# Kernel optimization log

Hardware: AMD Instinct MI355X
Metric: run time of the kernel (lower is better)

Reference implementation:

```python
import jax, jax.numpy as jnp
import numpy as np
from jax import lax

COMMITMENT_WEIGHT = 0.25
EMA_DECAY = 0.99
EPS = 1e-5


def setup_inputs() -> dict:
    key = jax.random.key(0)
    k1, k2, k3 = jax.random.split(key, 3)
    B, L, D, K = 32, 512, 384, 8192
    z = jax.random.normal(k1, (B, L, D), dtype=jnp.float32)
    codebook = jax.random.normal(k2, (K, D), dtype=jnp.float32)
    ema_cluster_size = jnp.zeros((K,), dtype=jnp.float32)
    ema_embed_sum = jax.random.normal(k3, (K, D), dtype=jnp.float32)
    return {"z": z, "codebook": codebook, "ema_cluster_size": ema_cluster_size, "ema_embed_sum": ema_embed_sum}


def reference(z, codebook, ema_cluster_size, ema_embed_sum):
    B, L, D = z.shape
    K = codebook.shape[0]
    flat_z = z.reshape(-1, D)  # [N, D]

    # squared L2 distance to every code: [N, K]
    dist = (
        jnp.sum(flat_z * flat_z, axis=-1, keepdims=True)
        + jnp.sum(codebook * codebook, axis=-1)[None, :]
        - 2.0 * (flat_z @ codebook.T)
    )
    indices = jnp.argmin(dist, axis=-1)  # [N]
    quantized = codebook[indices].reshape(B, L, D)

    # EMA codebook update (training-mode, no-grad in original)
    cluster_size = jax.ops.segment_sum(jnp.ones_like(indices, dtype=flat_z.dtype), indices, num_segments=K)
    embed_sum = jax.ops.segment_sum(flat_z, indices, num_segments=K)  # [K, D]
    new_cluster_size = ema_cluster_size * EMA_DECAY + (1.0 - EMA_DECAY) * cluster_size
    new_embed_sum = ema_embed_sum * EMA_DECAY + (1.0 - EMA_DECAY) * embed_sum
    n = jnp.sum(new_cluster_size)
    cluster_size_smoothed = (new_cluster_size + EPS) / (n + K * EPS) * n
    new_codebook = new_embed_sum / cluster_size_smoothed[:, None]

    commitment_loss = jnp.mean((z - lax.stop_gradient(quantized)) ** 2)
    codebook_loss = jnp.mean((quantized - lax.stop_gradient(z)) ** 2)
    loss = codebook_loss + COMMITMENT_WEIGHT * commitment_loss

    # straight-through estimator
    quantized_st = z + lax.stop_gradient(quantized - z)
    return (quantized_st, indices.reshape(B, L), loss, new_cluster_size, new_embed_sum, new_codebook)
```

## Files before the change

kernel.cpp:

```cpp
#include <hip/hip_runtime.h>
#include <math.h>

#define N_TOK 16384
#define DDIM  384
#define KCODE 8192
#define EMA   0.99f
#define EPS_F 1e-5f
#define MARGIN 0.5f
#define NB 32

typedef _Float16 f16x8 __attribute__((ext_vector_type(8)));
typedef float    f32x4 __attribute__((ext_vector_type(4)));

#define OFF_PD1    0UL
#define OFF_PI1    2097152UL
#define OFF_PD2    4194304UL
#define OFF_CBH    6291456UL
#define OFF_TOKL   0UL
#define OFF_OFFS   65536UL
#define OFF_CURS   98560UL
#define OFF_WSIDX  12582912UL
#define OFF_COUNTS 12648448UL
#define OFF_SUMSQ  12681216UL
#define OFF_NACC   12681220UL
#define OFF_CNORM  12681472UL
#define OFF_FLIST  12714240UL
#define OFF_FCNT   12779776UL
#define OFF_PSUM   12780032UL
#define OFF_FD1    12796416UL

typedef __attribute__((address_space(1))) const unsigned int gas_uint;
typedef __attribute__((address_space(3))) unsigned int       las_uint;
__device__ __forceinline__ void gload_lds16(const void* g, void* l) {
    __builtin_amdgcn_global_load_lds((gas_uint*)g, (las_uint*)l, 16, 0, 0);
}

__global__ void convert_norm_kernel(const float* __restrict__ z, const float* __restrict__ cb,
                                    _Float16* __restrict__ zh, _Float16* __restrict__ cbh,
                                    float* __restrict__ cnorm) {
    int row  = (blockIdx.x * blockDim.x + threadIdx.x) >> 6;
    int lane = threadIdx.x & 63;
    const float* src;
    _Float16* dst;
    bool is_cb = (row >= N_TOK);
    if (is_cb) { int k = row - N_TOK; src = cb + (size_t)k * DDIM; dst = cbh + (size_t)k * DDIM; }
    else       {                      src = z  + (size_t)row * DDIM; dst = zh + (size_t)row * DDIM; }
    float s = 0.f;
    #pragma unroll
    for (int r = 0; r < 3; r++) {
        int e = (lane + 64 * r) * 2;
        float2 v = *(const float2*)(src + e);
        s = fmaf(v.x, v.x, fmaf(v.y, v.y, s));
        _Float16 h0 = (_Float16)v.x, h1 = (_Float16)v.y;
        dst[e] = h0; dst[e + 1] = h1;
    }
    if (is_cb) {
        #pragma unroll
        for (int off = 32; off > 0; off >>= 1) s += __shfl_down(s, off, 64);
        if (lane == 0) cnorm[row - N_TOK] = s;
    }
}

__launch_bounds__(512, 4)
__global__ void argmin16_kernel(const _Float16* __restrict__ zh, const _Float16* __restrict__ cbh,
                                const float* __restrict__ cnorm,
                                float* __restrict__ pd1, int* __restrict__ pi1,
                                float* __restrict__ pd2) {
    __shared__ _Float16 As[128 * 64];
    __shared__ _Float16 Bs[256 * 64];

    const int tid  = threadIdx.x;
    const int lane = tid & 63;
    const int wv   = tid >> 6;
    const int wy   = wv >> 2;
    const int wx   = wv & 3;
    const int m0   = blockIdx.x * 128;
    const int n0   = blockIdx.y * 256;
    const int l15  = lane & 15;
    const int l4   = lane >> 4;
    const int rsw  = l15 & 7;

    f32x4 acc[4][4];
    #pragma unroll
    for (int i = 0; i < 4; i++)
        #pragma unroll
        for (int j = 0; j < 4; j++) acc[i][j] = (f32x4){0.f, 0.f, 0.f, 0.f};

    const int r8  = lane >> 3;
    const int jch = (lane & 7) ^ (r8 & 7);
    const _Float16* a_g = zh  + (size_t)(m0 + wv * 8 + r8) * DDIM + jch * 8;
    const _Float16* b_g = cbh + (size_t)(n0 + wv * 8 + r8) * DDIM + jch * 8;
    _Float16* a_d = As + wv * 512;
    _Float16* b_d = Bs + wv * 512;

    gload_lds16(a_g,                      a_d);
    gload_lds16(a_g + (size_t)64 * DDIM,  a_d + 4096);
    gload_lds16(b_g,                      b_d);
    gload_lds16(b_g + (size_t)64 * DDIM,  b_d + 4096);
    gload_lds16(b_g + (size_t)128 * DDIM, b_d + 8192);
    gload_lds16(b_g + (size_t)192 * DDIM, b_d + 12288);

    for (int it = 0; it < 6; it++) {
        __syncthreads();
        f16x8 af[4], bf[4];
        #pragma unroll
        for (int im = 0; im < 4; im++)
            af[im] = *(const f16x8*)(As + (wy * 64 + im * 16 + l15) * 64 + (l4 ^ rsw) * 8);
        #pragma unroll
        for (int in = 0; in < 4; in++)
            bf[in] = *(const f16x8*)(Bs + (wx * 64 + in * 16 + l15) * 64 + (l4 ^ rsw) * 8);
        #pragma unroll
        for (int im = 0; im < 4; im++)
            #pragma unroll
            for (int in = 0; in < 4; in++)
                acc[im][in] = __builtin_amdgcn_mfma_f32_16x16x32_f16(af[im], bf[in], acc[im][in], 0, 0, 0);
        #pragma unroll
        for (int im = 0; im < 4; im++)
            af[im] = *(const f16x8*)(As + (wy * 64 + im * 16 + l15) * 64 + ((4 + l4) ^ rsw) * 8);
        #pragma unroll
        for (int in = 0; in < 4; in++)
            bf[in] = *(const f16x8*)(Bs + (wx * 64 + in * 16 + l15) * 64 + ((4 + l4) ^ rsw) * 8);
        __syncthreads();
        if (it < 5) {
            int kc = (it + 1) * 64;
            gload_lds16(a_g + kc,                      a_d);
            gload_lds16(a_g + (size_t)64 * DDIM + kc,  a_d + 4096);
            gload_lds16(b_g + kc,                      b_d);
            gload_lds16(b_g + (size_t)64 * DDIM + kc,  b_d + 4096);
            gload_lds16(b_g + (size_t)128 * DDIM + kc, b_d + 8192);
            gload_lds16(b_g + (size_t)192 * DDIM + kc, b_d + 12288);
        }
        #pragma unroll
        for (int im = 0; im < 4; im++)
            #pragma unroll
            for (int in = 0; in < 4; in++)
                acc[im][in] = __builtin_amdgcn_mfma_f32_16x16x32_f16(af[im], bf[in], acc[im][in], 0, 0, 0);
    }

    float* xd1 = (float*)&As[0];
    float* xd2 = xd1 + 512;
    int*   xi1 = (int*)(xd1 + 1024);

    float cn[4]; int cid[4];
    #pragma unroll
    for (int in = 0; in < 4; in++) {
        cid[in] = n0 + wx * 64 + in * 16 + l15;
        cn[in] = cnorm[cid[in]];
    }
    #pragma unroll
    for (int im = 0; im < 4; im++) {
        #pragma unroll
        for (int reg = 0; reg < 4; reg++) {
            float d1 = cn[0] - 2.f * acc[im][0][reg];
            int   i1 = cid[0];
            float d2 = 3.4e38f;
            #pragma unroll
            for (int in = 1; in < 4; in++) {
                float dd = cn[in] - 2.f * acc[im][in][reg];
                if (dd < d1) { d2 = d1; d1 = dd; i1 = cid[in]; }
                else d2 = fminf(d2, dd);
            }
            #pragma unroll
            for (int off = 1; off < 16; off <<= 1) {
                float od1 = __shfl_xor(d1, off, 16);
                int   oi1 = __shfl_xor(i1, off, 16);
                float od2 = __shfl_xor(d2, off, 16);
                if (od1 < d1 || (od1 == d1 && oi1 < i1)) { d2 = fminf(d1, od2); d1 = od1; i1 = oi1; }
                else d2 = fminf(d2, od1);
            }
            if (l15 == 0) {
                int tl = wy * 64 + im * 16 + l4 * 4 + reg;
                xd1[tl * 4 + wx] = d1; xi1[tl * 4 + wx] = i1; xd2[tl * 4 + wx] = d2;
            }
        }
    }
    __syncthreads();
    if (tid < 128) {
        float d1 = xd1[tid * 4], d2 = xd2[tid * 4];
        int   i1 = xi1[tid * 4];
        #pragma unroll
        for (int x = 1; x < 4; x++) {
            float od1 = xd1[tid * 4 + x], od2 = xd2[tid * 4 + x];
            int   oi1 = xi1[tid * 4 + x];
            if (od1 < d1 || (od1 == d1 && oi1 < i1)) { d2 = fminf(d1, od2); d1 = od1; i1 = oi1; }
            else d2 = fminf(d2, od1);
        }
        size_t o = (size_t)blockIdx.y * N_TOK + m0 + tid;
        pd1[o] = d1; pi1[o] = i1; pd2[o] = d2;
    }
}

__global__ void topmerge_kernel(const float* __restrict__ pd1, const int* __restrict__ pi1,
                                const float* __restrict__ pd2,
                                int* __restrict__ ws_idx, float* __restrict__ out_idx,
                                int* __restrict__ fcnt, int* __restrict__ flist,
                                float* __restrict__ fd1) {
    int t = blockIdx.x * blockDim.x + threadIdx.x;
    if (t >= N_TOK) return;
    float d1 = pd1[t], d2 = pd2[t];
    int   i1 = pi1[t];
    for (int nb = 1; nb < NB; nb++) {
        size_t o = (size_t)nb * N_TOK + t;
        float od1 = pd1[o], od2 = pd2[o];
        int   oi1 = pi1[o];
        if (od1 < d1 || (od1 == d1 && oi1 < i1)) { d2 = fminf(d1, od2); d1 = od1; i1 = oi1; }
        else d2 = fminf(d2, od1);
    }
    ws_idx[t] = i1;
    out_idx[t] = (float)i1;
    fd1[t] = d1;
    if (d2 - d1 < MARGIN) {
        int s = atomicAdd(fcnt, 1);
        flist[s] = t;
    }
}

__launch_bounds__(256)
__global__ void rescore2_kernel(const float* __restrict__ z, const float* __restrict__ cb,
                                const float* __restrict__ cnorm,
                                const float* __restrict__ pd1, const float* __restrict__ fd1,
                                const int* __restrict__ flist, const int* __restrict__ fcnt,
                                int* __restrict__ ws_idx, float* __restrict__ out_idx) {
    __shared__ float zt[4 * 384];
    const int lane = threadIdx.x & 63;
    const int wv   = threadIdx.x >> 6;
    const int count = fcnt[0];
    float* zrow = zt + wv * 384;
    for (int slot = blockIdx.x * 4 + wv; slot < count; slot += 2048 * 4) {
        int t = flist[slot];
        const float* zr = z + (size_t)t * DDIM;
        #pragma unroll
        for (int r = 0; r < 6; r++) zrow[lane + 64 * r] = zr[lane + 64 * r];
        float band = fd1[t] + MARGIN;
        float bd = 3.4e38f; int bi = 0x7fffffff;
        for (int nb = 0; nb < NB; nb++) {
            if (pd1[(size_t)nb * N_TOK + t] >= band) continue;
            #pragma unroll
            for (int c4 = 0; c4 < 4; c4++) {
                int c = nb * 256 + c4 * 64 + lane;
                const float* cr = cb + (size_t)c * DDIM;
                float a = 0.f;
                for (int d4 = 0; d4 < 96; d4++) {
                    float4 cv = *(const float4*)(cr + d4 * 4);
                    float4 zv = *(const float4*)(zrow + d4 * 4);
                    a = fmaf(zv.x, cv.x, a);
                    a = fmaf(zv.y, cv.y, a);
                    a = fmaf(zv.z, cv.z, a);
                    a = fmaf(zv.w, cv.w, a);
                }
                float dd = cnorm[c] - 2.f * a;
                if (dd < bd) { bd = dd; bi = c; }
            }
        }
        #pragma unroll
        for (int off = 32; off > 0; off >>= 1) {
            float od = __shfl_xor(bd, off, 64);
            int   oi = __shfl_xor(bi, off, 64);
            if (od < bd || (od == bd && oi < bi)) { bd = od; bi = oi; }
        }
        if (lane == 0) { ws_idx[t] = bi; out_idx[t] = (float)bi; }
    }
}

__global__ void quantize_kernel(const float* __restrict__ z, const float* __restrict__ cb,
                                const int* __restrict__ ws_idx,
                                float* __restrict__ out_q,
                                float* __restrict__ counts, float* __restrict__ psum) {
    __shared__ float sm[4];
    int t = (blockIdx.x * blockDim.x + threadIdx.x) >> 6;
    int lane = threadIdx.x & 63, wv = threadIdx.x >> 6;
    int k = ws_idx[t];
    const float* zr = z + (size_t)t * DDIM;
    const float* cr = cb + (size_t)k * DDIM;
    float* qr = out_q + (size_t)t * DDIM;
    float s = 0.f;
    #pragma unroll
    for (int r = 0; r < 6; r++) {
        int d = lane + 64 * r;
        float zv = zr[d];
        float qv = cr[d];
        qr[d] = qv;
        float df = zv - qv;
        s += df * df;
    }
    #pragma unroll
    for (int off = 32; off > 0; off >>= 1) s += __shfl_down(s, off, 64);
    if (lane == 0) {
        sm[wv] = s;
        atomicAdd(counts + k, 1.0f);
    }
    __syncthreads();
    if (threadIdx.x == 0) psum[blockIdx.x] = sm[0] + sm[1] + sm[2] + sm[3];
}

__global__ void scan_kernel(const float* __restrict__ counts,
                            int* __restrict__ offs, int* __restrict__ curs) {
    __shared__ int ps[1024];
    const int t = threadIdx.x;
    const int base = t * 8;
    int loc[8]; int s = 0;
    #pragma unroll
    for (int i = 0; i < 8; i++) { int c = (int)(counts[base + i] + 0.5f); loc[i] = s; s += c; }
    ps[t] = s;
    __syncthreads();
    for (int off = 1; off < 1024; off <<= 1) {
        int v = ps[t];
        int add = (t >= off) ? ps[t - off] : 0;
        __syncthreads();
        ps[t] = v + add;
        __syncthreads();
    }
    int excl = (t == 0) ? 0 : ps[t - 1];
    #pragma unroll
    for (int i = 0; i < 8; i++) {
        int o = excl + loc[i];
        offs[base + i] = o;
        curs[base + i] = o;
    }
    if (t == 1023) offs[KCODE] = ps[1023];
}

__global__ void fill_kernel(const int* __restrict__ ws_idx,
                            int* __restrict__ curs, int* __restrict__ toklist) {
    int t = blockIdx.x * blockDim.x + threadIdx.x;
    if (t >= N_TOK) return;
    int k = ws_idx[t];
    int slot = atomicAdd(curs + k, 1);
    toklist[slot] = t;
}

__global__ void cluster_kernel(const float* __restrict__ ema_cs, const float* __restrict__ counts,
                               float* __restrict__ out_ncs, float* __restrict__ n_acc,
                               const float* __restrict__ psum, float* __restrict__ out_loss) {
    int i = blockIdx.x * blockDim.x + threadIdx.x;
    float v = 0.f;
    if (i < KCODE) {
        v = EMA * ema_cs[i] + (1.f - EMA) * counts[i];
        out_ncs[i] = v;
    }
    __shared__ float sm[4];
    __shared__ float sm2[4];
    int lane = threadIdx.x & 63, w = threadIdx.x >> 6;
    #pragma unroll
    for (int off = 32; off > 0; off >>= 1) v += __shfl_down(v, off, 64);
    if (lane == 0) sm[w] = v;
    __syncthreads();
    if (threadIdx.x == 0) atomicAdd(n_acc, sm[0] + sm[1] + sm[2] + sm[3]);
    if (blockIdx.x == 0) {
        float s = 0.f;
        for (int j = threadIdx.x; j < 4096; j += 256) s += psum[j];
        #pragma unroll
        for (int off = 32; off > 0; off >>= 1) s += __shfl_down(s, off, 64);
        if (lane == 0) sm2[w] = s;
        __syncthreads();
        if (threadIdx.x == 0)
            out_loss[0] = 1.25f * (sm2[0] + sm2[1] + sm2[2] + sm2[3]) / (float)(N_TOK * DDIM);
    }
}

__global__ void codebook_fused_kernel(const float* __restrict__ z,
                                      const int* __restrict__ offs, const int* __restrict__ toklist,
                                      const float* __restrict__ ema_es,
                                      const float* __restrict__ ncs, const float* __restrict__ n_acc,
                                      float* __restrict__ out_es, float* __restrict__ out_cb) {
    int k = (blockIdx.x * blockDim.x + threadIdx.x) >> 6;
    int lane = threadIdx.x & 63;
    if (k >= KCODE) return;
    int o0 = offs[k], o1 = offs[k + 1];
    float sum[6] = {0.f, 0.f, 0.f, 0.f, 0.f, 0.f};
    for (int s = o0; s < o1; s++) {
        int tok = toklist[s];
        const float* zr = z + (size_t)tok * DDIM;
        #pragma unroll
        for (int r = 0; r < 6; r++) sum[r] += zr[lane + 64 * r];
    }
    float n = n_acc[0];
    float smooth = (ncs[k] + EPS_F) / (n + (float)KCODE * EPS_F) * n;
    float inv = 1.f / smooth;
    const float* er = ema_es + (size_t)k * DDIM;
    float* oes = out_es + (size_t)k * DDIM;
    float* ocb = out_cb + (size_t)k * DDIM;
    #pragma unroll
    for (int r = 0; r < 6; r++) {
        int d = lane + 64 * r;
        float es = EMA * er[d] + (1.f - EMA) * sum[r];
        oes[d] = es;
        ocb[d] = es * inv;
    }
}

extern "C" void kernel_launch(void* const* d_in, const int* in_sizes, int n_in,
                              void* d_out, int out_size, void* d_ws, size_t ws_size,
                              hipStream_t stream) {
    const float* z       = (const float*)d_in[0];
    const float* cb      = (const float*)d_in[1];
    const float* ema_cs  = (const float*)d_in[2];
    const float* ema_es  = (const float*)d_in[3];

    float* out      = (float*)d_out;
    float* out_q    = out;
    float* out_idx  = out + 6291456;
    float* out_loss = out + 6307840;
    float* out_ncs  = out + 6307841;
    float* out_es   = out + 6316033;
    float* out_cb   = out + 9461761;

    char* w = (char*)d_ws;
    float* pd1    = (float*)(w + OFF_PD1);
    int*   pi1    = (int*)  (w + OFF_PI1);
    float* pd2    = (float*)(w + OFF_PD2);
    _Float16* cbh = (_Float16*)(w + OFF_CBH);
    int*   toklist= (int*)  (w + OFF_TOKL);
    int*   offs   = (int*)  (w + OFF_OFFS);
    int*   curs   = (int*)  (w + OFF_CURS);
    float* cnorm  = (float*)(w + OFF_CNORM);
    int*   flist  = (int*)  (w + OFF_FLIST);
    int*   fcnt   = (int*)  (w + OFF_FCNT);
    int*   ws_idx = (int*)  (w + OFF_WSIDX);
    float* counts = (float*)(w + OFF_COUNTS);
    float* psum   = (float*)(w + OFF_PSUM);
    float* n_acc  = (float*)(w + OFF_NACC);
    float* fd1    = (float*)(w + OFF_FD1);

    _Float16* zh = (_Float16*)out;

    hipMemsetAsync(w + OFF_FCNT, 0, 256, stream);
    hipMemsetAsync(w + OFF_COUNTS, 0, 32768 + 256, stream);

    convert_norm_kernel<<<(N_TOK + KCODE) / 4, 256, 0, stream>>>(z, cb, zh, cbh, cnorm);

    dim3 grid_am(N_TOK / 128, KCODE / 256, 1);
    argmin16_kernel<<<grid_am, 512, 0, stream>>>(zh, cbh, cnorm, pd1, pi1, pd2);

    topmerge_kernel<<<N_TOK / 256, 256, 0, stream>>>(pd1, pi1, pd2, ws_idx, out_idx, fcnt, flist, fd1);

    rescore2_kernel<<<2048, 256, 0, stream>>>(z, cb, cnorm, pd1, fd1, flist, fcnt, ws_idx, out_idx);

    quantize_kernel<<<N_TOK * 64 / 256, 256, 0, stream>>>(z, cb, ws_idx, out_q, counts, psum);
    scan_kernel<<<1, 1024, 0, stream>>>(counts, offs, curs);
    fill_kernel<<<N_TOK / 256, 256, 0, stream>>>(ws_idx, curs, toklist);
    cluster_kernel<<<(KCODE + 255) / 256, 256, 0, stream>>>(ema_cs, counts, out_ncs, n_acc, psum, out_loss);
    codebook_fused_kernel<<<KCODE * 64 / 256, 256, 0, stream>>>(z, offs, toklist, ema_es, out_ncs, n_acc, out_es, out_cb);
}
```

Measured before the change: 572.0 us.

## Replace second-best tracking with near-tie flag; fuse memsets and cluster into existing kernels

The argmin GEMM epilogue no longer carries a second-best distance through the shuffle reductions. It computes a per-block flag (via ballot) marking tokens whose other candidates fall within the margin, and topmerge uses that flag to decide which tokens to rescore. The two memsets move into the convert kernel, and the cluster/loss kernel is folded into the single-block scan kernel, removing launches. This lightens the epilogue, but the flag is coarser than the old second-best test and may send more tokens to rescoring.

Measured after the change: 550.7 us. 3.7% less time.

```diff
diff --git a/kernel.cpp b/kernel.cpp
--- a/kernel.cpp
+++ b/kernel.cpp
@@ -14,7 +14,7 @@
 
 #define OFF_PD1    0UL
 #define OFF_PI1    2097152UL
-#define OFF_PD2    4194304UL
+#define OFF_PFL    4194304UL
 #define OFF_CBH    6291456UL
 #define OFF_TOKL   0UL
 #define OFF_OFFS   65536UL
@@ -37,7 +37,12 @@
 
 __global__ void convert_norm_kernel(const float* __restrict__ z, const float* __restrict__ cb,
                                     _Float16* __restrict__ zh, _Float16* __restrict__ cbh,
-                                    float* __restrict__ cnorm) {
+                                    float* __restrict__ cnorm,
+                                    float* __restrict__ zero_cnts, int* __restrict__ fcnt) {
+    if (blockIdx.x == 0) {
+        for (int i = threadIdx.x; i < 8256; i += 256) zero_cnts[i] = 0.f;
+        if (threadIdx.x < 64) fcnt[threadIdx.x] = 0;
+    }
     int row  = (blockIdx.x * blockDim.x + threadIdx.x) >> 6;
     int lane = threadIdx.x & 63;
     const float* src;
@@ -65,7 +70,7 @@
 __global__ void argmin16_kernel(const _Float16* __restrict__ zh, const _Float16* __restrict__ cbh,
                                 const float* __restrict__ cnorm,
                                 float* __restrict__ pd1, int* __restrict__ pi1,
-                                float* __restrict__ pd2) {
+                                int* __restrict__ pfl) {
     __shared__ _Float16 As[128 * 64];
     __shared__ _Float16 Bs[256 * 64];
 
@@ -138,7 +143,7 @@
     }
 
     float* xd1 = (float*)&As[0];
-    float* xd2 = xd1 + 512;
+    int*   xfl = (int*)(xd1 + 512);
     int*   xi1 = (int*)(xd1 + 1024);
 
     float cn[4]; int cid[4];
@@ -151,65 +156,67 @@
     for (int im = 0; im < 4; im++) {
         #pragma unroll
         for (int reg = 0; reg < 4; reg++) {
-            float d1 = cn[0] - 2.f * acc[im][0][reg];
-            int   i1 = cid[0];
-            float d2 = 3.4e38f;
-            #pragma unroll
-            for (int in = 1; in < 4; in++) {
-                float dd = cn[in] - 2.f * acc[im][in][reg];
-                if (dd < d1) { d2 = d1; d1 = dd; i1 = cid[in]; }
-                else d2 = fminf(d2, dd);
+            float dd[4];
+            #pragma unroll
+            for (int in = 0; in < 4; in++) dd[in] = cn[in] - 2.f * acc[im][in][reg];
+            float d1 = dd[0]; int i1 = cid[0];
+            #pragma unroll
+            for (int in = 1; in < 4; in++)
+                if (dd[in] < d1) { d1 = dd[in]; i1 = cid[in]; }
+            #pragma unroll
+            for (int off = 1; off < 16; off <<= 1) {
+                float od = __shfl_xor(d1, off, 16);
+                int   oi = __shfl_xor(i1, off, 16);
+                if (od < d1 || (od == d1 && oi < i1)) { d1 = od; i1 = oi; }
             }
-            #pragma unroll
-            for (int off = 1; off < 16; off <<= 1) {
-                float od1 = __shfl_xor(d1, off, 16);
-                int   oi1 = __shfl_xor(i1, off, 16);
-                float od2 = __shfl_xor(d2, off, 16);
-                if (od1 < d1 || (od1 == d1 && oi1 < i1)) { d2 = fminf(d1, od2); d1 = od1; i1 = oi1; }
-                else d2 = fminf(d2, od1);
-            }
+            bool fl = false;
+            #pragma unroll
+            for (int in = 0; in < 4; in++) fl |= (dd[in] < d1 + MARGIN) && (cid[in] != i1);
+            unsigned long long bal = __ballot(fl);
+            int gf = ((bal >> (l4 * 16)) & 0xFFFFULL) != 0ULL;
             if (l15 == 0) {
                 int tl = wy * 64 + im * 16 + l4 * 4 + reg;
-                xd1[tl * 4 + wx] = d1; xi1[tl * 4 + wx] = i1; xd2[tl * 4 + wx] = d2;
+                xd1[tl * 4 + wx] = d1; xi1[tl * 4 + wx] = i1; xfl[tl * 4 + wx] = gf;
             }
         }
     }
     __syncthreads();
     if (tid < 128) {
-        float d1 = xd1[tid * 4], d2 = xd2[tid * 4];
-        int   i1 = xi1[tid * 4];
+        float d1 = xd1[tid * 4]; int i1 = xi1[tid * 4]; int fl = xfl[tid * 4];
         #pragma unroll
         for (int x = 1; x < 4; x++) {
-            float od1 = xd1[tid * 4 + x], od2 = xd2[tid * 4 + x];
-            int   oi1 = xi1[tid * 4 + x];
-            if (od1 < d1 || (od1 == d1 && oi1 < i1)) { d2 = fminf(d1, od2); d1 = od1; i1 = oi1; }
-            else d2 = fminf(d2, od1);
+            float od = xd1[tid * 4 + x]; int oi = xi1[tid * 4 + x]; int ofl = xfl[tid * 4 + x];
+            if (od < d1 || (od == d1 && oi < i1)) { d1 = od; i1 = oi; fl = ofl; }
+        }
+        #pragma unroll
+        for (int x = 0; x < 4; x++) {
+            float od = xd1[tid * 4 + x]; int oi = xi1[tid * 4 + x];
+            fl |= (oi != i1 && od < d1 + MARGIN) ? 1 : 0;
         }
         size_t o = (size_t)blockIdx.y * N_TOK + m0 + tid;
-        pd1[o] = d1; pi1[o] = i1; pd2[o] = d2;
+        pd1[o] = d1; pi1[o] = i1; pfl[o] = fl;
     }
 }
 
 __global__ void topmerge_kernel(const float* __restrict__ pd1, const int* __restrict__ pi1,
-                                const float* __restrict__ pd2,
+                                const int* __restrict__ pfl,
                                 int* __restrict__ ws_idx, float* __restrict__ out_idx,
                                 int* __restrict__ fcnt, int* __restrict__ flist,
                                 float* __restrict__ fd1) {
     int t = blockIdx.x * blockDim.x + threadIdx.x;
     if (t >= N_TOK) return;
-    float d1 = pd1[t], d2 = pd2[t];
-    int   i1 = pi1[t];
+    float d1 = pd1[t]; int i1 = pi1[t]; int fl = pfl[t];
+    float d2 = 3.4e38f;
     for (int nb = 1; nb < NB; nb++) {
         size_t o = (size_t)nb * N_TOK + t;
-        float od1 = pd1[o], od2 = pd2[o];
-        int   oi1 = pi1[o];
-        if (od1 < d1 || (od1 == d1 && oi1 < i1)) { d2 = fminf(d1, od2); d1 = od1; i1 = oi1; }
+        float od1 = pd1[o]; int oi1 = pi1[o]; int ofl = pfl[o];
+        if (od1 < d1 || (od1 == d1 && oi1 < i1)) { d2 = fminf(d2, d1); d1 = od1; i1 = oi1; fl = ofl; }
         else d2 = fminf(d2, od1);
     }
     ws_idx[t] = i1;
     out_idx[t] = (float)i1;
     fd1[t] = d1;
-    if (d2 - d1 < MARGIN) {
+    if (fl || (d2 - d1 < MARGIN)) {
         int s = atomicAdd(fcnt, 1);
         flist[s] = t;
     }
@@ -293,14 +300,19 @@
     if (threadIdx.x == 0) psum[blockIdx.x] = sm[0] + sm[1] + sm[2] + sm[3];
 }
 
-__global__ void scan_kernel(const float* __restrict__ counts,
-                            int* __restrict__ offs, int* __restrict__ curs) {
+__global__ void scan_cluster_kernel(const float* __restrict__ counts,
+                                    const float* __restrict__ ema_cs,
+                                    const float* __restrict__ psum,
+                                    int* __restrict__ offs, int* __restrict__ curs,
+                                    float* __restrict__ out_ncs, float* __restrict__ n_acc,
+                                    float* __restrict__ out_loss) {
     __shared__ int ps[1024];
+    __shared__ float red[32];
     const int t = threadIdx.x;
     const int base = t * 8;
-    int loc[8]; int s = 0;
-    #pragma unroll
-    for (int i = 0; i < 8; i++) { int c = (int)(counts[base + i] + 0.5f); loc[i] = s; s += c; }
+    int loc[8]; int s = 0; float cf[8];
+    #pragma unroll
+    for (int i = 0; i < 8; i++) { cf[i] = counts[base + i]; int c = (int)(cf[i] + 0.5f); loc[i] = s; s += c; }
     ps[t] = s;
     __syncthreads();
     for (int off = 1; off < 1024; off <<= 1) {
@@ -318,6 +330,27 @@
         curs[base + i] = o;
     }
     if (t == 1023) offs[KCODE] = ps[1023];
+    float vs = 0.f;
+    #pragma unroll
+    for (int i = 0; i < 8; i++) {
+        float v = EMA * ema_cs[base + i] + (1.f - EMA) * cf[i];
+        out_ncs[base + i] = v;
+        vs += v;
+    }
+    float ls = 0.f;
+    for (int j = t; j < 4096; j += 1024) ls += psum[j];
+    int lane = t & 63, w = t >> 6;
+    #pragma unroll
+    for (int off = 32; off > 0; off >>= 1) { vs += __shfl_down(vs, off, 64); ls += __shfl_down(ls, off, 64); }
+    if (lane == 0) { red[w] = vs; red[16 + w] = ls; }
+    __syncthreads();
+    if (t == 0) {
+        float n = 0.f, l = 0.f;
+        #pragma unroll
+        for (int w2 = 0; w2 < 16; w2++) { n += red[w2]; l += red[16 + w2]; }
+        n_acc[0] = n;
+        out_loss[0] = 1.25f * l / (float)(N_TOK * DDIM);
+    }
 }
 
 __global__ void fill_kernel(const int* __restrict__ ws_idx,
@@ -327,35 +360,6 @@
     int k = ws_idx[t];
     int slot = atomicAdd(curs + k, 1);
     toklist[slot] = t;
-}
-
-__global__ void cluster_kernel(const float* __restrict__ ema_cs, const float* __restrict__ counts,
-                               float* __restrict__ out_ncs, float* __restrict__ n_acc,
-                               const float* __restrict__ psum, float* __restrict__ out_loss) {
-    int i = blockIdx.x * blockDim.x + threadIdx.x;
-    float v = 0.f;
-    if (i < KCODE) {
-        v = EMA * ema_cs[i] + (1.f - EMA) * counts[i];
-        out_ncs[i] = v;
-    }
-    __shared__ float sm[4];
-    __shared__ float sm2[4];
-    int lane = threadIdx.x & 63, w = threadIdx.x >> 6;
-    #pragma unroll
-    for (int off = 32; off > 0; off >>= 1) v += __shfl_down(v, off, 64);
-    if (lane == 0) sm[w] = v;
-    __syncthreads();
-    if (threadIdx.x == 0) atomicAdd(n_acc, sm[0] + sm[1] + sm[2] + sm[3]);
-    if (blockIdx.x == 0) {
-        float s = 0.f;
-        for (int j = threadIdx.x; j < 4096; j += 256) s += psum[j];
-        #pragma unroll
-        for (int off = 32; off > 0; off >>= 1) s += __shfl_down(s, off, 64);
-        if (lane == 0) sm2[w] = s;
-        __syncthreads();
-        if (threadIdx.x == 0)
-            out_loss[0] = 1.25f * (sm2[0] + sm2[1] + sm2[2] + sm2[3]) / (float)(N_TOK * DDIM);
-    }
 }
 
 __global__ void codebook_fused_kernel(const float* __restrict__ z,
@@ -408,7 +412,7 @@
     char* w = (char*)d_ws;
     float* pd1    = (float*)(w + OFF_PD1);
     int*   pi1    = (int*)  (w + OFF_PI1);
-    float* pd2    = (float*)(w + OFF_PD2);
+    int*   pfl    = (int*)  (w + OFF_PFL);
     _Float16* cbh = (_Float16*)(w + OFF_CBH);
     int*   toklist= (int*)  (w + OFF_TOKL);
     int*   offs   = (int*)  (w + OFF_OFFS);
@@ -424,21 +428,17 @@
 
     _Float16* zh = (_Float16*)out;
 
-    hipMemsetAsync(w + OFF_FCNT, 0, 256, stream);
-    hipMemsetAsync(w + OFF_COUNTS, 0, 32768 + 256, stream);
-
-    convert_norm_kernel<<<(N_TOK + KCODE) / 4, 256, 0, stream>>>(z, cb, zh, cbh, cnorm);
+    convert_norm_kernel<<<(N_TOK + KCODE) / 4, 256, 0, stream>>>(z, cb, zh, cbh, cnorm, counts, fcnt);
 
     dim3 grid_am(N_TOK / 128, KCODE / 256, 1);
-    argmin16_kernel<<<grid_am, 512, 0, stream>>>(zh, cbh, cnorm, pd1, pi1, pd2);
-
-    topmerge_kernel<<<N_TOK / 256, 256, 0, stream>>>(pd1, pi1, pd2, ws_idx, out_idx, fcnt, flist, fd1);
+    argmin16_kernel<<<grid_am, 512, 0, stream>>>(zh, cbh, cnorm, pd1, pi1, pfl);
+
+    topmerge_kernel<<<N_TOK / 256, 256, 0, stream>>>(pd1, pi1, pfl, ws_idx, out_idx, fcnt, flist, fd1);
 
     rescore2_kernel<<<2048, 256, 0, stream>>>(z, cb, cnorm, pd1, fd1, flist, fcnt, ws_idx, out_idx);
 
     quantize_kernel<<<N_TOK * 64 / 256, 256, 0, stream>>>(z, cb, ws_idx, out_q, counts, psum);
-    scan_kernel<<<1, 1024, 0, stream>>>(counts, offs, curs);
+    scan_cluster_kernel<<<1, 1024, 0, stream>>>(counts, ema_cs, psum, offs, curs, out_ncs, n_acc, out_loss);
     fill_kernel<<<N_TOK / 256, 256, 0, stream>>>(ws_idx, curs, toklist);
-    cluster_kernel<<<(KCODE + 255) / 256, 256, 0, stream>>>(ema_cs, counts, out_ncs, n_acc, psum, out_loss);
     codebook_fused_kernel<<<KCODE * 64 / 256, 256, 0, stream>>>(z, offs, toklist, ema_es, out_ncs, n_acc, out_es, out_cb);
 }
```
